# Kernel optimization log

Hardware: AMD Instinct MI355X
Metric: run time of the kernel (lower is better)

Reference implementation:

```python
import jax, jax.numpy as jnp
import numpy as np

N_NODES = 100000
N_EDGES = 1600000
N_GRAPHS = 128
CONV = [64, 64, 64]
HID = [256, 128, 2]
GFT = 64
EPS = 1e-5
NEG_SLOPE = 0.01


def leaky_relu(x):
    return jnp.where(x >= 0, x, NEG_SLOPE * x)


def setup_inputs() -> dict:
    key = jax.random.key(0)
    ks = jax.random.split(key, 32)
    inp = {}
    inp['x'] = jax.random.normal(ks[0], (N_NODES, CONV[0]), dtype=jnp.float32)
    inp['edge_index'] = jax.random.randint(ks[1], (2, N_EDGES), 0, N_NODES, dtype=jnp.int64)
    inp['graph_features'] = jax.random.normal(ks[2], (N_GRAPHS, GFT), dtype=jnp.float32)
    inp['batch'] = jnp.sort(jax.random.randint(ks[3], (N_NODES,), 0, N_GRAPHS, dtype=jnp.int64))
    # SAGEConv params per layer: W_l (aggregated branch, with bias), W_r (root branch), BN gamma/beta
    ki = 4
    for li in range(len(CONV) - 1):
        fin, fout = CONV[li], CONV[li + 1]
        s = 1.0 / np.sqrt(fin)
        inp[f'Wl{li}'] = jax.random.uniform(ks[ki], (fin, fout), minval=-s, maxval=s); ki += 1
        inp[f'bl{li}'] = jax.random.uniform(ks[ki], (fout,), minval=-s, maxval=s); ki += 1
        inp[f'Wr{li}'] = jax.random.uniform(ks[ki], (fin, fout), minval=-s, maxval=s); ki += 1
        inp[f'g{li}'] = jnp.ones((fout,), jnp.float32)
        inp[f'b{li}'] = jnp.zeros((fout,), jnp.float32)
    # MLP: Linear(128->256), LeakyReLU, Linear(256->128), LeakyReLU, Linear(128->2)
    dims = [CONV[-1] + GFT] + HID
    for li in range(len(HID)):
        fin, fout = dims[li], dims[li + 1]
        s = 1.0 / np.sqrt(fin)
        inp[f'Wm{li}'] = jax.random.uniform(ks[ki], (fin, fout), minval=-s, maxval=s); ki += 1
        inp[f'bm{li}'] = jax.random.uniform(ks[ki], (fout,), minval=-s, maxval=s); ki += 1
    return inp


def _sage_block(x, src, dst, Wl, bl, Wr, gamma, beta):
    # PyG SAGEConv (aggr='mean'): out = lin_l(mean_{j in N(i)} x_j) + lin_r(x_i)
    msgs = x[src]                                               # [E, Fin] gather
    agg = jax.ops.segment_sum(msgs, dst, num_segments=N_NODES)  # [N, Fin] scatter-add
    deg = jax.ops.segment_sum(jnp.ones((src.shape[0],), x.dtype), dst, num_segments=N_NODES)
    agg = agg / jnp.maximum(deg, 1.0)[:, None]
    h = agg @ Wl + bl + x @ Wr
    h = leaky_relu(h)
    # BatchNorm1d (training mode: batch stats over nodes, biased variance)
    mu = h.mean(axis=0)
    var = h.var(axis=0)
    return (h - mu) * jax.lax.rsqrt(var + EPS) * gamma + beta


def reference(x, edge_index, graph_features, batch,
              Wl0, bl0, Wr0, g0, b0, Wl1, bl1, Wr1, g1, b1,
              Wm0, bm0, Wm1, bm1, Wm2, bm2):
    src, dst = edge_index[0], edge_index[1]
    h = _sage_block(x, src, dst, Wl0, bl0, Wr0, g0, b0)
    h = _sage_block(h, src, dst, Wl1, bl1, Wr1, g1, b1)
    # scatter_mean graph pooling
    pooled = jax.ops.segment_sum(h, batch, num_segments=N_GRAPHS)
    cnt = jax.ops.segment_sum(jnp.ones((h.shape[0],), h.dtype), batch, num_segments=N_GRAPHS)
    pooled = pooled / jnp.maximum(cnt, 1.0)[:, None]
    z = jnp.concatenate([pooled, graph_features], axis=1)       # [G, 128]
    z = leaky_relu(z @ Wm0 + bm0)
    z = leaky_relu(z @ Wm1 + bm1)
    return z @ Wm2 + bm2
```

## Files before the change

kernel.cpp:

```cpp
#include <hip/hip_runtime.h>

#define N_NODES 100000
#define N_EDGES 1600000
#define N_GRAPHS 128
#define FDIM 64
#define EPSV 1e-5f
#define NEG 0.01f

#define NB 782
#define PART_BLOCKS 391
#define NTILES 6250
#define TPB 8
#define GEMM_BLOCKS 782

typedef short bf16x8 __attribute__((ext_vector_type(8)));
typedef float f32x4  __attribute__((ext_vector_type(4)));

__device__ __forceinline__ float leaky(float x){ return x >= 0.f ? x : NEG*x; }

__device__ __forceinline__ unsigned short f2bf(float x){
    unsigned u = __float_as_uint(x);
    return (unsigned short)((u + 0x7fffu + ((u >> 16) & 1u)) >> 16);
}
__device__ __forceinline__ float bf2f(unsigned short b){
    return __uint_as_float(((unsigned)b) << 16);
}

__global__ __launch_bounds__(256) void k_cvt(const float* __restrict__ x,
                                             unsigned short* __restrict__ o){
    int i = blockIdx.x*256 + threadIdx.x;
    if (i < (N_NODES*FDIM)/4){
        float4 v = ((const float4*)x)[i];
        ushort4 r;
        r.x = f2bf(v.x); r.y = f2bf(v.y); r.z = f2bf(v.z); r.w = f2bf(v.w);
        ((ushort4*)o)[i] = r;
    }
}

__global__ __launch_bounds__(256) void k_bh(const int* __restrict__ dst, int* __restrict__ bhist){
    __shared__ int lh[NB];
    int t = threadIdx.x;
    for (int i = t; i < NB; i += 256) lh[i] = 0;
    __syncthreads();
    int base = blockIdx.x * 4096;
    #pragma unroll
    for (int k = 0; k < 16; ++k){
        int e = base + k*256 + t;
        if (e < N_EDGES) atomicAdd(&lh[dst[e] >> 7], 1);
    }
    __syncthreads();
    for (int i = t; i < NB; i += 256) if (lh[i]) atomicAdd(&bhist[i], lh[i]);
}

__global__ __launch_bounds__(256) void k_bscan(const int* __restrict__ bhist,
                                               int* __restrict__ boff, int* __restrict__ cur){
    __shared__ int lds[256];
    int t = threadIdx.x;
    int base = t*4;
    int v0 = (base+0 < NB) ? bhist[base+0] : 0;
    int v1 = (base+1 < NB) ? bhist[base+1] : 0;
    int v2 = (base+2 < NB) ? bhist[base+2] : 0;
    int v3 = (base+3 < NB) ? bhist[base+3] : 0;
    lds[t] = v0+v1+v2+v3; __syncthreads();
    for (int off = 1; off < 256; off <<= 1){
        int add = (t >= off) ? lds[t-off] : 0; __syncthreads();
        lds[t] += add; __syncthreads();
    }
    int excl = (t > 0) ? lds[t-1] : 0;
    int p0 = excl, p1 = excl+v0, p2 = excl+v0+v1, p3 = excl+v0+v1+v2;
    if (base+0 < NB){ boff[base+0] = p0; cur[base+0] = p0; }
    if (base+1 < NB){ boff[base+1] = p1; cur[base+1] = p1; }
    if (base+2 < NB){ boff[base+2] = p2; cur[base+2] = p2; }
    if (base+3 < NB){ boff[base+3] = p3; cur[base+3] = p3; }
    if (t == 0) boff[NB] = N_EDGES;
}

__global__ __launch_bounds__(256) void k_part(const int* __restrict__ src, const int* __restrict__ dst,
                                              int* __restrict__ cur, int* __restrict__ packed){
    __shared__ int lh[NB];
    __shared__ int lc[NB];
    int t = threadIdx.x;
    for (int i = t; i < NB; i += 256) lh[i] = 0;
    __syncthreads();
    int base = blockIdx.x * 4096;
    int d[16];
    #pragma unroll
    for (int k = 0; k < 16; ++k){
        int e = base + k*256 + t;
        d[k] = (e < N_EDGES) ? dst[e] : -1;
        if (d[k] >= 0) atomicAdd(&lh[d[k] >> 7], 1);
    }
    __syncthreads();
    for (int i = t; i < NB; i += 256) lc[i] = atomicAdd(&cur[i], lh[i]);
    __syncthreads();
    #pragma unroll
    for (int k = 0; k < 16; ++k){
        int e = base + k*256 + t;
        if (e < N_EDGES){
            int b = d[k] >> 7;
            int p = atomicAdd(&lc[b], 1);
            packed[p] = (src[e] << 7) | (d[k] & 127);
        }
    }
}

__global__ __launch_bounds__(256) void k_sort(const int* __restrict__ packed,
                                              const int* __restrict__ boff,
                                              int* __restrict__ rs, int* __restrict__ col){
    __shared__ int hist[128];
    __shared__ int curs[128];
    int b = blockIdx.x, t = threadIdx.x;
    int e0 = boff[b], e1 = boff[b+1];
    if (t < 128) hist[t] = 0;
    __syncthreads();
    for (int e = e0 + t; e < e1; e += 256)
        atomicAdd(&hist[packed[e] & 127], 1);
    __syncthreads();
    int cnt = (t < 128) ? hist[t] : 0;
    __syncthreads();
    for (int off = 1; off < 128; off <<= 1){
        int add = (t < 128 && t >= off) ? hist[t-off] : 0;
        __syncthreads();
        if (t < 128) hist[t] += add;
        __syncthreads();
    }
    int nbase = b << 7;
    int nloc = min(128, N_NODES - nbase);
    if (t < nloc){
        int excl = hist[t] - cnt;
        rs[nbase + t] = e0 + excl;
        curs[t] = excl;
    }
    __syncthreads();
    for (int e = e0 + t; e < e1; e += 256){
        int v = packed[e];
        int p = atomicAdd(&curs[v & 127], 1);
        col[e0 + p] = ((unsigned)v) >> 7;
    }
    if (b == 0 && t == 0) rs[N_NODES] = N_EDGES;
}

__global__ __launch_bounds__(256) void k_agg(
    const unsigned short* __restrict__ xin, const int* __restrict__ rs,
    const int* __restrict__ col, unsigned short* __restrict__ agg)
{
    int t = threadIdx.x;
    int lane = t & 63;
    int sub = lane >> 4;
    int q   = lane & 15;
    int wid = (blockIdx.x << 2) + (t >> 6);
    const int nw = gridDim.x << 2;
    for (int n = wid; n < N_NODES; n += nw){
        int e0 = __builtin_amdgcn_readfirstlane(rs[n]);
        int e1 = __builtin_amdgcn_readfirstlane(rs[n+1]);
        float ax=0.f, ay=0.f, az=0.f, aw=0.f;
        for (int e = e0; e < e1; e += 16){
            int i0 = e + sub, i1 = e + 4 + sub, i2 = e + 8 + sub, i3 = e + 12 + sub;
            if (i0 < e1){
                uint2 u = ((const uint2*)(xin + ((size_t)col[i0] << 6)))[q];
                ax += __uint_as_float(u.x << 16); ay += __uint_as_float(u.x & 0xffff0000u);
                az += __uint_as_float(u.y << 16); aw += __uint_as_float(u.y & 0xffff0000u);
            }
            if (i1 < e1){
                uint2 u = ((const uint2*)(xin + ((size_t)col[i1] << 6)))[q];
                ax += __uint_as_float(u.x << 16); ay += __uint_as_float(u.x & 0xffff0000u);
                az += __uint_as_float(u.y << 16); aw += __uint_as_float(u.y & 0xffff0000u);
            }
            if (i2 < e1){
                uint2 u = ((const uint2*)(xin + ((size_t)col[i2] << 6)))[q];
                ax += __uint_as_float(u.x << 16); ay += __uint_as_float(u.x & 0xffff0000u);
                az += __uint_as_float(u.y << 16); aw += __uint_as_float(u.y & 0xffff0000u);
            }
            if (i3 < e1){
                uint2 u = ((const uint2*)(xin + ((size_t)col[i3] << 6)))[q];
                ax += __uint_as_float(u.x << 16); ay += __uint_as_float(u.x & 0xffff0000u);
                az += __uint_as_float(u.y << 16); aw += __uint_as_float(u.y & 0xffff0000u);
            }
        }
        ax += __shfl_xor(ax, 16, 64); ay += __shfl_xor(ay, 16, 64);
        az += __shfl_xor(az, 16, 64); aw += __shfl_xor(aw, 16, 64);
        ax += __shfl_xor(ax, 32, 64); ay += __shfl_xor(ay, 32, 64);
        az += __shfl_xor(az, 32, 64); aw += __shfl_xor(aw, 32, 64);
        if (sub == 0){
            float rd = 1.f / fmaxf((float)(e1 - e0), 1.f);
            ushort4 o;
            o.x = f2bf(ax*rd); o.y = f2bf(ay*rd);
            o.z = f2bf(az*rd); o.w = f2bf(aw*rd);
            ((ushort4*)(agg + ((size_t)n << 6)))[q] = o;
        }
    }
}

template<bool AFF>
__global__ __launch_bounds__(256) void k_gemm(
    const unsigned short* __restrict__ agg,
    const unsigned short* __restrict__ xin,
    unsigned short* __restrict__ hout,
    const int* __restrict__ rs, const int* __restrict__ batch,
    const float* __restrict__ Wl, const float* __restrict__ Wr,
    const float* __restrict__ scale,
    const float* __restrict__ bbias, const float* __restrict__ bdelta,
    float* __restrict__ bnpart, float* __restrict__ S)
{
    __shared__ float sS[8*64];
    int t = threadIdx.x;
    int lane = t & 63;
    int jt = t >> 6;
    int g = lane >> 4, r = lane & 15;
    int j = (jt << 4) + r;

    bf16x8 wlh[2], wll[2], wrh[2], wrl[2];
    #pragma unroll
    for (int ks = 0; ks < 2; ++ks){
        #pragma unroll
        for (int i = 0; i < 8; ++i){
            int k = (ks << 5) + (g << 3) + i;
            float s = AFF ? scale[k] : 1.f;
            float wv = Wl[(k << 6) + j] * s;
            unsigned u = __float_as_uint(wv);
            wlh[ks][i] = (short)(u >> 16);
            float lf = wv - __uint_as_float(u & 0xffff0000u);
            wll[ks][i] = (short)(__float_as_uint(lf) >> 16);
            wv = Wr[(k << 6) + j] * s;
            u = __float_as_uint(wv);
            wrh[ks][i] = (short)(u >> 16);
            lf = wv - __uint_as_float(u & 0xffff0000u);
            wrl[ks][i] = (short)(__float_as_uint(lf) >> 16);
        }
    }

    float bb = bbias[j];
    float bd = AFF ? bdelta[j] : 0.f;

    int gbase = 0, span = 0;
    if (AFF){
        for (int i = t; i < 512; i += 256) sS[i] = 0.f;
        int nfirst = blockIdx.x * (TPB*16);
        int nlast  = min(nfirst + TPB*16 - 1, N_NODES - 1);
        gbase = batch[nfirst];
        span  = batch[nlast] - gbase + 1;
        __syncthreads();
    }

    float bs = 0.f, bq = 0.f;
    int c0 = blockIdx.x * TPB;
    int cend = min(c0 + TPB, NTILES);

    auto LOADT = [&](int tile, bf16x8* A, bf16x8* X, int4& R, int& R5, int4& B){
        size_t rowoff = (((size_t)((tile << 4) + r)) << 6) + (g << 3);
        const bf16x8* pa = (const bf16x8*)(agg + rowoff);
        const bf16x8* px = (const bf16x8*)(xin + rowoff);
        A[0] = pa[0]; A[1] = pa[4];
        X[0] = px[0]; X[1] = px[4];
        if (AFF){
            int nb = (tile << 4) + (g << 2);
            R  = *(const int4*)(rs + nb);
            R5 = rs[nb + 4];
            B  = *(const int4*)(batch + nb);
        }
    };

    auto POOL = [&](int gr, float hv){
        int lg = gr - gbase;
        if (lg < 8) atomicAdd(&sS[(lg << 6) + j], hv);
        else        atomicAdd(&S[(gr << 6) + j], hv);
    };

    auto COMPUTE = [&](int tile, const bf16x8* A, const bf16x8* X,
                       const int4& R, int R5, const int4& B){
        f32x4 accA = {0.f, 0.f, 0.f, 0.f};
        f32x4 accX = {0.f, 0.f, 0.f, 0.f};
        accA = __builtin_amdgcn_mfma_f32_16x16x32_bf16(A[0], wlh[0], accA, 0, 0, 0);
        accA = __builtin_amdgcn_mfma_f32_16x16x32_bf16(A[0], wll[0], accA, 0, 0, 0);
        accA = __builtin_amdgcn_mfma_f32_16x16x32_bf16(A[1], wlh[1], accA, 0, 0, 0);
        accA = __builtin_amdgcn_mfma_f32_16x16x32_bf16(A[1], wll[1], accA, 0, 0, 0);
        accX = __builtin_amdgcn_mfma_f32_16x16x32_bf16(X[0], wrh[0], accX, 0, 0, 0);
        accX = __builtin_amdgcn_mfma_f32_16x16x32_bf16(X[0], wrl[0], accX, 0, 0, 0);
        accX = __builtin_amdgcn_mfma_f32_16x16x32_bf16(X[1], wrh[1], accX, 0, 0, 0);
        accX = __builtin_amdgcn_mfma_f32_16x16x32_bf16(X[1], wrl[1], accX, 0, 0, 0);

        int nb = (tile << 4) + (g << 2);
        if (AFF){
            float hv;
            hv = accA[0] + accX[0] + bb + ((R.y - R.x) > 0 ? bd : 0.f);
            hv = leaky(hv); bs += hv; bq += hv*hv; POOL(B.x, hv);
            hv = accA[1] + accX[1] + bb + ((R.z - R.y) > 0 ? bd : 0.f);
            hv = leaky(hv); bs += hv; bq += hv*hv; POOL(B.y, hv);
            hv = accA[2] + accX[2] + bb + ((R.w - R.z) > 0 ? bd : 0.f);
            hv = leaky(hv); bs += hv; bq += hv*hv; POOL(B.z, hv);
            hv = accA[3] + accX[3] + bb + ((R5 - R.w) > 0 ? bd : 0.f);
            hv = leaky(hv); bs += hv; bq += hv*hv; POOL(B.w, hv);
        } else {
            #pragma unroll
            for (int q = 0; q < 4; ++q){
                float hv = leaky(accA[q] + accX[q] + bb);
                unsigned short h16 = f2bf(hv);
                float hr = bf2f(h16);
                hout[((size_t)(nb + q) << 6) + j] = h16;
                bs += hr; bq += hr*hr;
            }
        }
    };

    bf16x8 Aa[2], Xa[2], Ab[2], Xb[2];
    int4 Ra = {0,0,0,0}, Rb = {0,0,0,0}, Ba = {0,0,0,0}, Bb = {0,0,0,0};
    int R5a = 0, R5b = 0;

    LOADT(c0, Aa, Xa, Ra, R5a, Ba);
    for (int c = c0; c < cend; c += 2){
        if (c + 1 < cend) LOADT(c + 1, Ab, Xb, Rb, R5b, Bb);
        COMPUTE(c, Aa, Xa, Ra, R5a, Ba);
        if (c + 2 < cend) LOADT(c + 2, Aa, Xa, Ra, R5a, Ba);
        if (c + 1 < cend) COMPUTE(c + 1, Ab, Xb, Rb, R5b, Bb);
    }

    bs += __shfl_xor(bs, 16, 64); bs += __shfl_xor(bs, 32, 64);
    bq += __shfl_xor(bq, 16, 64); bq += __shfl_xor(bq, 32, 64);
    if (lane < 16){
        float* bp = bnpart + ((blockIdx.x & 31) * 128);
        atomicAdd(&bp[(jt << 4) + lane], bs);
        atomicAdd(&bp[64 + (jt << 4) + lane], bq);
    }

    if (AFF){
        __syncthreads();
        int sp = min(span, 8);
        for (int i = t; i < (sp << 6); i += 256){
            float v = sS[i];
            if (v != 0.f) atomicAdd(&S[((gbase + (i >> 6)) << 6) + (i & 63)], v);
        }
    }
}

template<bool FOLD>
__global__ __launch_bounds__(64) void k_bnfin(
    const float* __restrict__ bnpart,
    const float* __restrict__ gamma, const float* __restrict__ beta,
    const float* __restrict__ Wl_nx, const float* __restrict__ Wr_nx,
    const float* __restrict__ bl_nx,
    float* __restrict__ scale, float* __restrict__ shift,
    float* __restrict__ bbias, float* __restrict__ bdelta)
{
    __shared__ float ssh[64];
    int j = threadIdx.x;
    float s = 0.f, q = 0.f;
    #pragma unroll 8
    for (int i = 0; i < 32; ++i){
        s += bnpart[i*128 + j];
        q += bnpart[i*128 + 64 + j];
    }
    float mu  = s * (1.0f/N_NODES);
    float var = q * (1.0f/N_NODES) - mu*mu;
    float sc  = gamma[j] * rsqrtf(var + EPSV);
    float sh  = beta[j] - mu*sc;
    scale[j] = sc; shift[j] = sh;
    if (FOLD){
        ssh[j] = sh;
        __syncthreads();
        float bbv = bl_nx[j], bdv = 0.f;
        #pragma unroll 8
        for (int k = 0; k < 64; ++k){
            bbv += ssh[k] * Wr_nx[(k << 6) + j];
            bdv += ssh[k] * Wl_nx[(k << 6) + j];
        }
        bbias[j] = bbv; bdelta[j] = bdv;
    }
}

__global__ __launch_bounds__(256) void k_mlp(
    const float* __restrict__ S, const int* __restrict__ batch,
    const float* __restrict__ scale, const float* __restrict__ shift,
    const float* __restrict__ gf,
    const float* __restrict__ Wm0, const float* __restrict__ bm0,
    const float* __restrict__ Wm1, const float* __restrict__ bm1,
    const float* __restrict__ Wm2, const float* __restrict__ bm2,
    float* __restrict__ out)
{
    __shared__ int seg[2];
    __shared__ float z[128];
    __shared__ float h1[256];
    __shared__ float h2[128];
    int g = blockIdx.x, t = threadIdx.x;
    if (t < 2){
        int target = g + t;
        int lo = 0, hi = N_NODES;
        while (lo < hi){ int mid = (lo+hi)>>1; if (batch[mid] < target) lo = mid+1; else hi = mid; }
        seg[t] = lo;
    }
    __syncthreads();
    float cnt = (float)(seg[1] - seg[0]);
    if (t < 64)
        z[t] = (scale[t]*S[(g<<6)+t] + cnt*shift[t]) / fmaxf(cnt, 1.f);
    else if (t < 128)
        z[t] = gf[g*64 + (t-64)];
    __syncthreads();
    float acc = bm0[t];
    #pragma unroll 8
    for (int k = 0; k < 128; ++k) acc += z[k]*Wm0[k*256 + t];
    h1[t] = leaky(acc);
    __syncthreads();
    if (t < 128){
        float a = bm1[t];
        #pragma unroll 8
        for (int k = 0; k < 256; ++k) a += h1[k]*Wm1[k*128 + t];
        h2[t] = leaky(a);
    }
    __syncthreads();
    if (t < 2){
        float a = bm2[t];
        for (int k = 0; k < 128; ++k) a += h2[k]*Wm2[k*2 + t];
        out[g*2 + t] = a;
    }
}

extern "C" void kernel_launch(void* const* d_in, const int* in_sizes, int n_in,
                              void* d_out, int out_size, void* d_ws, size_t ws_size,
                              hipStream_t stream) {
    const float* x     = (const float*)d_in[0];
    const int*   ei    = (const int*)d_in[1];
    const float* gf    = (const float*)d_in[2];
    const int*   batch = (const int*)d_in[3];
    const float* Wl0 = (const float*)d_in[4];
    const float* bl0 = (const float*)d_in[5];
    const float* Wr0 = (const float*)d_in[6];
    const float* g0  = (const float*)d_in[7];
    const float* b0  = (const float*)d_in[8];
    const float* Wl1 = (const float*)d_in[9];
    const float* bl1 = (const float*)d_in[10];
    const float* Wr1 = (const float*)d_in[11];
    const float* g1  = (const float*)d_in[12];
    const float* b1  = (const float*)d_in[13];
    const float* Wm0 = (const float*)d_in[14];
    const float* bm0 = (const float*)d_in[15];
    const float* Wm1 = (const float*)d_in[16];
    const float* bm1 = (const float*)d_in[17];
    const float* Wm2 = (const float*)d_in[18];
    const float* bm2 = (const float*)d_in[19];

    int*   bhist  = (int*)d_ws;
    int*   boff   = bhist + NB;
    int*   cur    = boff + NB + 1;
    int*   packed = (int*)d_ws + 2348;
    int*   rs     = packed + N_EDGES;
    int*   col    = rs + 100004;
    unsigned short* xbf   = (unsigned short*)(col + N_EDGES);
    unsigned short* h1bf  = xbf + (size_t)N_NODES*FDIM;
    unsigned short* aggbf = h1bf + (size_t)N_NODES*FDIM;
    float* bnpart = (float*)(aggbf + (size_t)N_NODES*FDIM);
    float* S      = bnpart + 4096;
    float* scale0 = S + N_GRAPHS*FDIM;
    float* shift0 = scale0 + 64;
    float* scale1 = scale0 + 128;
    float* shift1 = scale0 + 192;
    float* bbias  = scale0 + 256;
    float* bdelta = scale0 + 320;

    const int* srcp = ei;
    const int* dstp = ei + N_EDGES;

    hipMemsetAsync(bhist, 0, NB*sizeof(int), stream);
    k_cvt<<<(N_NODES*FDIM/4 + 255)/256, 256, 0, stream>>>(x, xbf);
    k_bh<<<PART_BLOCKS, 256, 0, stream>>>(dstp, bhist);
    k_bscan<<<1, 256, 0, stream>>>(bhist, boff, cur);
    k_part<<<PART_BLOCKS, 256, 0, stream>>>(srcp, dstp, cur, packed);
    k_sort<<<NB, 256, 0, stream>>>(packed, boff, rs, col);

    hipMemsetAsync(bnpart, 0, 4096*sizeof(float), stream);
    k_agg<<<2048, 256, 0, stream>>>(xbf, rs, col, aggbf);
    k_gemm<false><<<GEMM_BLOCKS, 256, 0, stream>>>(
        aggbf, xbf, h1bf, rs, batch,
        Wl0, Wr0, nullptr, bl0, nullptr, bnpart, nullptr);
    k_bnfin<true><<<1, 64, 0, stream>>>(bnpart, g0, b0, Wl1, Wr1, bl1,
                                        scale0, shift0, bbias, bdelta);

    hipMemsetAsync(bnpart, 0, (4096 + N_GRAPHS*FDIM)*sizeof(float), stream);
    k_agg<<<2048, 256, 0, stream>>>(h1bf, rs, col, aggbf);
    k_gemm<true><<<GEMM_BLOCKS, 256, 0, stream>>>(
        aggbf, h1bf, nullptr, rs, batch,
        Wl1, Wr1, scale0, bbias, bdelta, bnpart, S);
    k_bnfin<false><<<1, 64, 0, stream>>>(bnpart, g1, b1, nullptr, nullptr, nullptr,
                                         scale1, shift1, nullptr, nullptr);

    k_mlp<<<N_GRAPHS, 256, 0, stream>>>(S, batch, scale1, shift1, gf,
                                        Wm0, bm0, Wm1, bm1, Wm2, bm2, (float*)d_out);
}
```

Measured before the change: 284.9 us.

## Split aggregation into two feature-half passes and fuse prep/memset kernels

The neighbour-mean aggregation now runs as two passes, each gathering one 32-feature half (64 bytes) of every source row. Each wave covers 8 edges in parallel with 8 lanes per row, and column indices are stored pre-scaled as byte offsets. The smaller working set per pass is meant to improve cache hit rates on the random gathers, at the cost of reading the CSR indices twice and launching twice. The bf16 conversion and the bucket histogram are merged into one kernel, and the separate memsets are replaced by zeroing done inside existing kernels, which cuts launch overhead.

```diff
diff --git a/kernel.cpp b/kernel.cpp
--- a/kernel.cpp
+++ b/kernel.cpp
@@ -9,6 +9,7 @@
 
 #define NB 782
 #define PART_BLOCKS 391
+#define CVT_BLOCKS 1563
 #define NTILES 6250
 #define TPB 8
 #define GEMM_BLOCKS 782
@@ -26,30 +27,38 @@
     return __uint_as_float(((unsigned)b) << 16);
 }
 
-__global__ __launch_bounds__(256) void k_cvt(const float* __restrict__ x,
-                                             unsigned short* __restrict__ o){
-    int i = blockIdx.x*256 + threadIdx.x;
-    if (i < (N_NODES*FDIM)/4){
-        float4 v = ((const float4*)x)[i];
-        ushort4 r;
-        r.x = f2bf(v.x); r.y = f2bf(v.y); r.z = f2bf(v.z); r.w = f2bf(v.w);
-        ((ushort4*)o)[i] = r;
-    }
-}
-
-__global__ __launch_bounds__(256) void k_bh(const int* __restrict__ dst, int* __restrict__ bhist){
+__global__ __launch_bounds__(256) void k_prep(const float* __restrict__ x,
+                                              unsigned short* __restrict__ o,
+                                              const int* __restrict__ dst,
+                                              int* __restrict__ bhist,
+                                              float* __restrict__ bnpart){
     __shared__ int lh[NB];
-    int t = threadIdx.x;
-    for (int i = t; i < NB; i += 256) lh[i] = 0;
-    __syncthreads();
-    int base = blockIdx.x * 4096;
-    #pragma unroll
-    for (int k = 0; k < 16; ++k){
-        int e = base + k*256 + t;
-        if (e < N_EDGES) atomicAdd(&lh[dst[e] >> 7], 1);
-    }
-    __syncthreads();
-    for (int i = t; i < NB; i += 256) if (lh[i]) atomicAdd(&bhist[i], lh[i]);
+    int b = blockIdx.x, t = threadIdx.x;
+    if (b < CVT_BLOCKS){
+        int base = b*1024 + t;
+        #pragma unroll
+        for (int k2 = 0; k2 < 4; ++k2){
+            int i = base + k2*256;
+            if (i < (N_NODES*FDIM)/4){
+                float4 v = ((const float4*)x)[i];
+                ushort4 r;
+                r.x = f2bf(v.x); r.y = f2bf(v.y); r.z = f2bf(v.z); r.w = f2bf(v.w);
+                ((ushort4*)o)[i] = r;
+            }
+        }
+        if (b < 16) bnpart[(b << 8) + t] = 0.f;
+    } else {
+        for (int i = t; i < NB; i += 256) lh[i] = 0;
+        __syncthreads();
+        int base = (b - CVT_BLOCKS) * 4096;
+        #pragma unroll
+        for (int k = 0; k < 16; ++k){
+            int e = base + k*256 + t;
+            if (e < N_EDGES) atomicAdd(&lh[dst[e] >> 7], 1);
+        }
+        __syncthreads();
+        for (int i = t; i < NB; i += 256) if (lh[i]) atomicAdd(&bhist[i], lh[i]);
+    }
 }
 
 __global__ __launch_bounds__(256) void k_bscan(const int* __restrict__ bhist,
@@ -106,7 +115,7 @@
 
 __global__ __launch_bounds__(256) void k_sort(const int* __restrict__ packed,
                                               const int* __restrict__ boff,
-                                              int* __restrict__ rs, int* __restrict__ col){
+                                              int* __restrict__ rs, int* __restrict__ colb){
     __shared__ int hist[128];
     __shared__ int curs[128];
     int b = blockIdx.x, t = threadIdx.x;
@@ -135,48 +144,52 @@
     for (int e = e0 + t; e < e1; e += 256){
         int v = packed[e];
         int p = atomicAdd(&curs[v & 127], 1);
-        col[e0 + p] = ((unsigned)v) >> 7;
+        colb[e0 + p] = v & 0xFFFFFF80;
     }
     if (b == 0 && t == 0) rs[N_NODES] = N_EDGES;
 }
 
+template<int PASS>
 __global__ __launch_bounds__(256) void k_agg(
     const unsigned short* __restrict__ xin, const int* __restrict__ rs,
-    const int* __restrict__ col, unsigned short* __restrict__ agg)
+    const int* __restrict__ colb, unsigned short* __restrict__ agg)
 {
     int t = threadIdx.x;
     int lane = t & 63;
-    int sub = lane >> 4;
-    int q   = lane & 15;
+    int sub = lane >> 3;
+    int q   = lane & 7;
+    const char* xb = (const char*)xin + (PASS << 6) + (q << 3);
     int wid = (blockIdx.x << 2) + (t >> 6);
     const int nw = gridDim.x << 2;
     for (int n = wid; n < N_NODES; n += nw){
         int e0 = __builtin_amdgcn_readfirstlane(rs[n]);
         int e1 = __builtin_amdgcn_readfirstlane(rs[n+1]);
         float ax=0.f, ay=0.f, az=0.f, aw=0.f;
-        for (int e = e0; e < e1; e += 16){
-            int i0 = e + sub, i1 = e + 4 + sub, i2 = e + 8 + sub, i3 = e + 12 + sub;
-            if (i0 < e1){
-                uint2 u = ((const uint2*)(xin + ((size_t)col[i0] << 6)))[q];
+        for (int e = e0 + sub; e < e1; e += 32){
+            {
+                uint2 u = *(const uint2*)(xb + colb[e]);
                 ax += __uint_as_float(u.x << 16); ay += __uint_as_float(u.x & 0xffff0000u);
                 az += __uint_as_float(u.y << 16); aw += __uint_as_float(u.y & 0xffff0000u);
             }
+            int i1 = e + 8, i2 = e + 16, i3 = e + 24;
             if (i1 < e1){
-                uint2 u = ((const uint2*)(xin + ((size_t)col[i1] << 6)))[q];
+                uint2 u = *(const uint2*)(xb + colb[i1]);
                 ax += __uint_as_float(u.x << 16); ay += __uint_as_float(u.x & 0xffff0000u);
                 az += __uint_as_float(u.y << 16); aw += __uint_as_float(u.y & 0xffff0000u);
             }
             if (i2 < e1){
-                uint2 u = ((const uint2*)(xin + ((size_t)col[i2] << 6)))[q];
+                uint2 u = *(const uint2*)(xb + colb[i2]);
                 ax += __uint_as_float(u.x << 16); ay += __uint_as_float(u.x & 0xffff0000u);
                 az += __uint_as_float(u.y << 16); aw += __uint_as_float(u.y & 0xffff0000u);
             }
             if (i3 < e1){
-                uint2 u = ((const uint2*)(xin + ((size_t)col[i3] << 6)))[q];
+                uint2 u = *(const uint2*)(xb + colb[i3]);
                 ax += __uint_as_float(u.x << 16); ay += __uint_as_float(u.x & 0xffff0000u);
                 az += __uint_as_float(u.y << 16); aw += __uint_as_float(u.y & 0xffff0000u);
             }
         }
+        ax += __shfl_xor(ax, 8, 64); ay += __shfl_xor(ay, 8, 64);
+        az += __shfl_xor(az, 8, 64); aw += __shfl_xor(aw, 8, 64);
         ax += __shfl_xor(ax, 16, 64); ay += __shfl_xor(ay, 16, 64);
         az += __shfl_xor(az, 16, 64); aw += __shfl_xor(aw, 16, 64);
         ax += __shfl_xor(ax, 32, 64); ay += __shfl_xor(ay, 32, 64);
@@ -186,7 +199,7 @@
             ushort4 o;
             o.x = f2bf(ax*rd); o.y = f2bf(ay*rd);
             o.z = f2bf(az*rd); o.w = f2bf(aw*rd);
-            ((ushort4*)(agg + ((size_t)n << 6)))[q] = o;
+            *(ushort4*)((char*)agg + (((size_t)n) << 7) + (PASS << 6) + (q << 3)) = o;
         }
     }
 }
@@ -334,12 +347,13 @@
 
 template<bool FOLD>
 __global__ __launch_bounds__(64) void k_bnfin(
-    const float* __restrict__ bnpart,
+    float* __restrict__ bnpart,
     const float* __restrict__ gamma, const float* __restrict__ beta,
     const float* __restrict__ Wl_nx, const float* __restrict__ Wr_nx,
     const float* __restrict__ bl_nx,
     float* __restrict__ scale, float* __restrict__ shift,
-    float* __restrict__ bbias, float* __restrict__ bdelta)
+    float* __restrict__ bbias, float* __restrict__ bdelta,
+    float* __restrict__ Szero)
 {
     __shared__ float ssh[64];
     int j = threadIdx.x;
@@ -364,6 +378,9 @@
             bdv += ssh[k] * Wl_nx[(k << 6) + j];
         }
         bbias[j] = bbv; bdelta[j] = bdv;
+        __syncthreads();
+        for (int i = j; i < 4096; i += 64) bnpart[i] = 0.f;
+        for (int i = j; i < N_GRAPHS*FDIM; i += 64) Szero[i] = 0.f;
     }
 }
 
@@ -442,8 +459,8 @@
     int*   cur    = boff + NB + 1;
     int*   packed = (int*)d_ws + 2348;
     int*   rs     = packed + N_EDGES;
-    int*   col    = rs + 100004;
-    unsigned short* xbf   = (unsigned short*)(col + N_EDGES);
+    int*   colb   = rs + 100004;
+    unsigned short* xbf   = (unsigned short*)(colb + N_EDGES);
     unsigned short* h1bf  = xbf + (size_t)N_NODES*FDIM;
     unsigned short* aggbf = h1bf + (size_t)N_NODES*FDIM;
     float* bnpart = (float*)(aggbf + (size_t)N_NODES*FDIM);
@@ -459,27 +476,26 @@
     const int* dstp = ei + N_EDGES;
 
     hipMemsetAsync(bhist, 0, NB*sizeof(int), stream);
-    k_cvt<<<(N_NODES*FDIM/4 + 255)/256, 256, 0, stream>>>(x, xbf);
-    k_bh<<<PART_BLOCKS, 256, 0, stream>>>(dstp, bhist);
+    k_prep<<<CVT_BLOCKS + PART_BLOCKS, 256, 0, stream>>>(x, xbf, dstp, bhist, bnpart);
     k_bscan<<<1, 256, 0, stream>>>(bhist, boff, cur);
     k_part<<<PART_BLOCKS, 256, 0, stream>>>(srcp, dstp, cur, packed);
-    k_sort<<<NB, 256, 0, stream>>>(packed, boff, rs, col);
-
-    hipMemsetAsync(bnpart, 0, 4096*sizeof(float), stream);
-    k_agg<<<2048, 256, 0, stream>>>(xbf, rs, col, aggbf);
+    k_sort<<<NB, 256, 0, stream>>>(packed, boff, rs, colb);
+
+    k_agg<0><<<2048, 256, 0, stream>>>(xbf, rs, colb, aggbf);
+    k_agg<1><<<2048, 256, 0, stream>>>(xbf, rs, colb, aggbf);
     k_gemm<false><<<GEMM_BLOCKS, 256, 0, stream>>>(
         aggbf, xbf, h1bf, rs, batch,
         Wl0, Wr0, nullptr, bl0, nullptr, bnpart, nullptr);
     k_bnfin<true><<<1, 64, 0, stream>>>(bnpart, g0, b0, Wl1, Wr1, bl1,
-                                        scale0, shift0, bbias, bdelta);
-
-    hipMemsetAsync(bnpart, 0, (4096 + N_GRAPHS*FDIM)*sizeof(float), stream);
-    k_agg<<<2048, 256, 0, stream>>>(h1bf, rs, col, aggbf);
+                                        scale0, shift0, bbias, bdelta, S);
+
+    k_agg<0><<<2048, 256, 0, stream>>>(h1bf, rs, colb, aggbf);
+    k_agg<1><<<2048, 256, 0, stream>>>(h1bf, rs, colb, aggbf);
     k_gemm<true><<<GEMM_BLOCKS, 256, 0, stream>>>(
         aggbf, h1bf, nullptr, rs, batch,
         Wl1, Wr1, scale0, bbias, bdelta, bnpart, S);
     k_bnfin<false><<<1, 64, 0, stream>>>(bnpart, g1, b1, nullptr, nullptr, nullptr,
-                                         scale1, shift1, nullptr, nullptr);
+                                         scale1, shift1, nullptr, nullptr, nullptr);
 
     k_mlp<<<N_GRAPHS, 256, 0, stream>>>(S, batch, scale1, shift1, gf,
                                         Wm0, bm0, Wm1, bm1, Wm2, bm2, (float*)d_out);
```

Result: slower. 306.7 us (+7.7%).
